# Performance work log

Measured on AMD Instinct MI355X. Metric: run time of the kernel, lower is better.

The kernel has to match this reference:

```python
import jax, jax.numpy as jnp
import numpy as np

B, S = 16, 4096
E_ENC, E_DEC, H = 1024, 1024, 512


def setup_inputs() -> dict:
    key = jax.random.key(0)
    ks = jax.random.split(key, 8)
    sc_e = 1.0 / np.sqrt(E_ENC)
    sc_d = 1.0 / np.sqrt(E_DEC)
    sc_h = 1.0 / np.sqrt(H)
    return {
        "encoder_hiddens": jax.random.normal(ks[0], (B, S, E_ENC), jnp.float32),
        "decoder_hidden": jax.random.normal(ks[1], (B, E_DEC), jnp.float32),
        "We": jax.random.uniform(ks[2], (E_ENC, H), jnp.float32, -sc_e, sc_e),
        "be": jax.random.uniform(ks[3], (H,), jnp.float32, -sc_e, sc_e),
        "Wd": jax.random.uniform(ks[4], (E_DEC, H), jnp.float32, -sc_d, sc_d),
        "bd": jax.random.uniform(ks[5], (H,), jnp.float32, -sc_d, sc_d),
        "Wo": jax.random.uniform(ks[6], (H, 1), jnp.float32, -sc_h, sc_h),
        "bo": jax.random.uniform(ks[7], (1,), jnp.float32, -sc_h, sc_h),
    }


def reference(encoder_hiddens, decoder_hidden, We, be, Wd, bd, Wo, bo):
    # Additive (Bahdanau) attention.
    # enc_proj: [B,S,H]; dec_proj: [B,1,H] broadcast over sequence.
    enc_proj = jnp.einsum("bse,eh->bsh", encoder_hiddens, We) + be
    dec_proj = jnp.einsum("bd,dh->bh", decoder_hidden, Wd) + bd
    e = jnp.tanh(enc_proj + dec_proj[:, None, :])          # [B,S,H]
    scores = jnp.einsum("bsh,h->bs", e, Wo[:, 0]) + bo[0]  # [B,S]
    attn = jax.nn.softmax(scores, axis=-1)                 # [B,S]
    context = jnp.einsum("bs,bse->be", attn, encoder_hiddens)  # [B,E_ENC]
    return context
```

## Files before the change

kernel.cpp:

```cpp
#include <hip/hip_runtime.h>
#include <hip/hip_bf16.h>
#include <math.h>

#define B_ 16
#define S_ 4096
#define E_ 1024
#define H_ 512

#define BM 128
#define BN 128
#define BK 64
#define NCHUNK (E_ / BK)

typedef short bf16x8 __attribute__((ext_vector_type(8)));
typedef unsigned short u16x8 __attribute__((ext_vector_type(8)));
typedef float f32x4 __attribute__((ext_vector_type(4)));

__device__ inline unsigned short f2bf(float x) {
    __hip_bfloat16 h = __float2bfloat16(x);
    return *(unsigned short*)&h;
}
__device__ inline float bf2f(unsigned short u) {
    unsigned int x = ((unsigned int)u) << 16;
    float f;
    __builtin_memcpy(&f, &x, 4);
    return f;
}
__device__ __forceinline__ void gld16(const unsigned short* g, unsigned short* l) {
    __builtin_amdgcn_global_load_lds(
        (const __attribute__((address_space(1))) void*)g,
        (__attribute__((address_space(3))) void*)l, 16, 0, 0);
}

__global__ __launch_bounds__(256) void prep_kernel(
    const float* __restrict__ We, const float* __restrict__ dec,
    const float* __restrict__ Wd, const float* __restrict__ bd,
    const float* __restrict__ be, unsigned short* __restrict__ WeTcB,
    float* __restrict__ dp) {
    __shared__ float red[4][64];
    int bid = blockIdx.x, t = threadIdx.x;
    if (bid < 64) {
        int c = bid >> 2, n0t = (bid & 3) * 128;
#pragma unroll 4
        for (int it = 0; it < 32; ++it) {
            int o = it * 256 + t;
            int n_rel = o >> 6, within = o & 63;
            int cp = within >> 3, j = within & 7;
            int n = n0t + n_rel;
            int k = c * 64 + ((cp ^ (n & 7)) << 3) + j;
            WeTcB[c * 32768 + n * 64 + within] = f2bf(We[(size_t)k * H_ + n]);
        }
    } else {
        int id = bid - 64;
        int b = id >> 3, hc = id & 7;
        int h = hc * 64 + (t & 63);
        int ec = t >> 6;
        const float* dr = dec + b * E_ + ec * 256;
        const float* wp = Wd + (size_t)(ec * 256) * H_ + h;
        float acc = 0.f;
#pragma unroll 8
        for (int e = 0; e < 256; ++e) acc = fmaf(dr[e], wp[(size_t)e * H_], acc);
        red[ec][t & 63] = acc;
        __syncthreads();
        if (t < 64) {
            int hh = hc * 64 + t;
            dp[b * H_ + hh] = red[0][t] + red[1][t] + red[2][t] + red[3][t] + bd[hh] + be[hh];
        }
    }
}

__global__ __launch_bounds__(256, 3) void scores_gemm_kernel(
    const float* __restrict__ enc, const unsigned short* __restrict__ WeTcB,
    const float* __restrict__ Wo, const float* __restrict__ dp,
    float* __restrict__ parts, unsigned short* __restrict__ encB) {
    __shared__ unsigned short sA[BM * BK];
    __shared__ unsigned short sB[BN * BK];
    __shared__ float sRed[2][BM];

    int tid = threadIdx.x;
    int w = tid >> 6, l = tid & 63;
    int l16 = l & 15, quad = l >> 4;
    int wm = w & 1, wn = w >> 1;
    int bid = blockIdx.x;
    int xcd = bid & 7;
    int sq = bid >> 3;
    int nt = sq & 3;
    size_t mt = (size_t)((sq >> 2) << 3) + xcd;
    size_t m0 = mt * BM;
    int n0 = nt * BN;
    int b = (int)(m0 >> 12);
    bool writeB = (nt == 0);

    int arowS = tid >> 3;
    int akb = tid & 7;
    const float* gAf = enc + (m0 + arowS) * E_ + akb * 8;
    unsigned short* sAw = sA + arowS * BK + ((akb ^ (arowS & 7)) << 3);
    unsigned short* encBw = encB + (m0 + arowS) * E_ + akb * 8;
    const unsigned short* gB = WeTcB + (size_t)n0 * BK + (w * 8) * BK + l * 8;
    unsigned short* sBb = sB + (w * 8) * BK;

    f32x4 acc[4][4];
#pragma unroll
    for (int i = 0; i < 4; ++i)
#pragma unroll
        for (int j = 0; j < 4; ++j) acc[i][j] = (f32x4)0.f;

    int arow = (wm * 64 + l16) * BK;
    int brow = (wn * 64 + l16) * BK;
    int sw = l16 & 7;

    for (int c = 0; c < NCHUNK; ++c) {
        __syncthreads();
        int k0 = c * BK;
#pragma unroll
        for (int i = 0; i < 4; ++i)
            gld16(gB + (size_t)c * (H_ * BK) + i * 32 * BK, sBb + i * 32 * BK);
#pragma unroll
        for (int it = 0; it < 4; ++it) {
            const float* p = gAf + (size_t)it * 32 * E_ + k0;
            float4 va = *(const float4*)(p);
            float4 vb = *(const float4*)(p + 4);
            u16x8 u;
            u[0] = f2bf(va.x); u[1] = f2bf(va.y); u[2] = f2bf(va.z); u[3] = f2bf(va.w);
            u[4] = f2bf(vb.x); u[5] = f2bf(vb.y); u[6] = f2bf(vb.z); u[7] = f2bf(vb.w);
            *(u16x8*)(sAw + it * 32 * BK) = u;
            if (writeB) *(u16x8*)(encBw + (size_t)it * 32 * E_ + k0) = u;
        }
        __syncthreads();
#pragma unroll
        for (int half = 0; half < 2; ++half) {
            int koff = (((half * 4 + quad) ^ sw) << 3);
            bf16x8 aR[4], bR[4];
#pragma unroll
            for (int i = 0; i < 4; ++i)
                aR[i] = *(const bf16x8*)(sA + arow + i * 16 * BK + koff);
#pragma unroll
            for (int j = 0; j < 4; ++j)
                bR[j] = *(const bf16x8*)(sB + brow + j * 16 * BK + koff);
#pragma unroll
            for (int i = 0; i < 4; ++i)
#pragma unroll
                for (int j = 0; j < 4; ++j)
                    acc[i][j] = __builtin_amdgcn_mfma_f32_16x16x32_bf16(aR[i], bR[j], acc[i][j], 0, 0, 0);
        }
    }

    float dpv[4], wov[4];
    const float* dpb = dp + b * H_;
#pragma unroll
    for (int j = 0; j < 4; ++j) {
        int h = n0 + wn * 64 + j * 16 + l16;
        dpv[j] = dpb[h];
        wov[j] = Wo[h];
    }
#pragma unroll
    for (int i = 0; i < 4; ++i)
#pragma unroll
        for (int r = 0; r < 4; ++r) {
            float s = 0.f;
#pragma unroll
            for (int j = 0; j < 4; ++j) {
                float x = acc[i][j][r] + dpv[j];
                float e = __expf(2.f * x);
                s += (1.f - 2.f / (e + 1.f)) * wov[j];
            }
            s += __shfl_xor(s, 1, 64);
            s += __shfl_xor(s, 2, 64);
            s += __shfl_xor(s, 4, 64);
            s += __shfl_xor(s, 8, 64);
            if (l16 == 0) sRed[wn][wm * 64 + i * 16 + quad * 4 + r] = s;
        }
    __syncthreads();
    if (tid < BM) {
        int s_in = (int)(m0 & (S_ - 1)) + tid;
        parts[(size_t)(nt * B_ + b) * S_ + s_in] = sRed[0][tid] + sRed[1][tid];
    }
}

__global__ __launch_bounds__(256) void stats_kernel(const float* __restrict__ parts,
                                                    float2* __restrict__ stats) {
    int b = blockIdx.x, tid = threadIdx.x;
    const float4* p0 = (const float4*)(parts + (size_t)(0 * B_ + b) * S_);
    const float4* p1 = (const float4*)(parts + (size_t)(1 * B_ + b) * S_);
    const float4* p2 = (const float4*)(parts + (size_t)(2 * B_ + b) * S_);
    const float4* p3 = (const float4*)(parts + (size_t)(3 * B_ + b) * S_);
    float4 v[4];
    float m = -1e30f;
#pragma unroll
    for (int i = 0; i < 4; ++i) {
        int idx = i * 256 + tid;
        float4 a0 = p0[idx], a1 = p1[idx], a2 = p2[idx], a3 = p3[idx];
        v[i].x = a0.x + a1.x + a2.x + a3.x;
        v[i].y = a0.y + a1.y + a2.y + a3.y;
        v[i].z = a0.z + a1.z + a2.z + a3.z;
        v[i].w = a0.w + a1.w + a2.w + a3.w;
        m = fmaxf(m, fmaxf(fmaxf(v[i].x, v[i].y), fmaxf(v[i].z, v[i].w)));
    }
    for (int off = 32; off; off >>= 1) m = fmaxf(m, __shfl_xor(m, off, 64));
    __shared__ float redm[4];
    __shared__ float reds[4];
    if ((tid & 63) == 0) redm[tid >> 6] = m;
    __syncthreads();
    m = fmaxf(fmaxf(redm[0], redm[1]), fmaxf(redm[2], redm[3]));
    float s = 0.f;
#pragma unroll
    for (int i = 0; i < 4; ++i) {
        s += __expf(v[i].x - m) + __expf(v[i].y - m);
        s += __expf(v[i].z - m) + __expf(v[i].w - m);
    }
    for (int off = 32; off; off >>= 1) s += __shfl_xor(s, off, 64);
    if ((tid & 63) == 0) reds[tid >> 6] = s;
    __syncthreads();
    if (tid == 0) {
        stats[b] = make_float2(m, reds[0] + reds[1] + reds[2] + reds[3]);
    }
}

__global__ __launch_bounds__(256) void ctx_partial_bf16(
    const unsigned short* __restrict__ encB, const float* __restrict__ parts,
    const float2* __restrict__ stats, float* __restrict__ part) {
    int b = blockIdx.x >> 5;
    int c = blockIdx.x & 31;
    int s0 = c * 128;
    int tid = threadIdx.x;
    __shared__ float w[128];
    if (tid < 128) {
        size_t idx = (size_t)b * S_ + s0 + tid;
        float x = parts[(size_t)(0 * B_) * S_ + idx] + parts[(size_t)(1 * B_) * S_ + idx] +
                  parts[(size_t)(2 * B_) * S_ + idx] + parts[(size_t)(3 * B_) * S_ + idx];
        w[tid] = __expf(x - stats[b].x);
    }
    __syncthreads();
    int e8 = (tid & 127) * 8;
    int sh = tid >> 7;
    const unsigned short* base = encB + ((size_t)b * S_ + s0 + sh * 64) * E_ + e8;
    const float* wp = w + sh * 64;
    float acc[8];
#pragma unroll
    for (int t = 0; t < 8; ++t) acc[t] = 0.f;
    for (int s = 0; s < 64; s += 8) {
        u16x8 v[8];
#pragma unroll
        for (int u = 0; u < 8; ++u) v[u] = *(const u16x8*)(base + (size_t)(s + u) * E_);
#pragma unroll
        for (int u = 0; u < 8; ++u) {
            float ws = wp[s + u];
#pragma unroll
            for (int t = 0; t < 8; ++t) acc[t] = fmaf(ws, bf2f(v[u][t]), acc[t]);
        }
    }
    float* po = part + ((size_t)(b * 64 + c * 2 + sh)) * E_ + e8;
    *(float4*)(po) = make_float4(acc[0], acc[1], acc[2], acc[3]);
    *(float4*)(po + 4) = make_float4(acc[4], acc[5], acc[6], acc[7]);
}

__global__ __launch_bounds__(256) void ctx_reduce(const float* __restrict__ part,
                                                  const float2* __restrict__ stats,
                                                  float* __restrict__ out) {
    int idx = blockIdx.x * 256 + threadIdx.x;
    int b = idx >> 10;
    int e = idx & 1023;
    const float* p = part + (size_t)b * 64 * E_ + e;
    float s0 = 0.f, s1 = 0.f, s2 = 0.f, s3 = 0.f;
    for (int c = 0; c < 64; c += 4) {
        s0 += p[(size_t)(c + 0) * E_];
        s1 += p[(size_t)(c + 1) * E_];
        s2 += p[(size_t)(c + 2) * E_];
        s3 += p[(size_t)(c + 3) * E_];
    }
    out[idx] = ((s0 + s1) + (s2 + s3)) * (1.f / stats[b].y);
}

extern "C" void kernel_launch(void* const* d_in, const int* in_sizes, int n_in,
                              void* d_out, int out_size, void* d_ws, size_t ws_size,
                              hipStream_t stream) {
    const float* enc = (const float*)d_in[0];
    const float* dec = (const float*)d_in[1];
    const float* We  = (const float*)d_in[2];
    const float* be  = (const float*)d_in[3];
    const float* Wd  = (const float*)d_in[4];
    const float* bd  = (const float*)d_in[5];
    const float* Wo  = (const float*)d_in[6];
    float* out = (float*)d_out;

    char* wsp = (char*)d_ws;
    unsigned short* WeTcB = (unsigned short*)wsp;
    float* dp = (float*)(wsp + (1 << 20));
    float2* stats = (float2*)(wsp + (1 << 20) + (32 << 10));
    float* parts = (float*)(wsp + (1 << 20) + (64 << 10));
    float* part = (float*)(wsp + (4 << 20));
    unsigned short* encB = (unsigned short*)(wsp + (8 << 20));

    prep_kernel<<<192, 256, 0, stream>>>(We, dec, Wd, bd, be, WeTcB, dp);
    scores_gemm_kernel<<<(B_ * S_ / BM) * (H_ / BN), 256, 0, stream>>>(
        enc, WeTcB, Wo, dp, parts, encB);
    stats_kernel<<<B_, 256, 0, stream>>>(parts, stats);
    ctx_partial_bf16<<<B_ * 32, 256, 0, stream>>>(encB, parts, stats, part);
    ctx_reduce<<<B_ * E_ / 256, 256, 0, stream>>>(part, stats, out);
}
```

Before: 514.2 us.

## Load fp32 encoder tiles directly to LDS, drop bf16 copy, fuse softmax stats

The GEMM now streams fp32 encoder tiles into LDS with global_load_lds, using an XOR-swizzled layout, and converts them to bf16 when reading fragments. This removes the register-staged conversion path and the bf16 side copy of the encoder. The context pass reads the fp32 encoder directly and computes per-chunk max and sum. The separate stats kernel is replaced by a chunked online-softmax rescale in ctx_reduce. The cost is double the LDS footprint for A, which may cut occupancy, and a second full fp32 read of the encoder in the context pass.

After: 489.3 us. 4.8% less time.

```diff
diff --git a/kernel.cpp b/kernel.cpp
--- a/kernel.cpp
+++ b/kernel.cpp
@@ -26,7 +26,7 @@
     __builtin_memcpy(&f, &x, 4);
     return f;
 }
-__device__ __forceinline__ void gld16(const unsigned short* g, unsigned short* l) {
+__device__ __forceinline__ void gld16(const void* g, void* l) {
     __builtin_amdgcn_global_load_lds(
         (const __attribute__((address_space(1))) void*)g,
         (__attribute__((address_space(3))) void*)l, 16, 0, 0);
@@ -72,8 +72,8 @@
 __global__ __launch_bounds__(256, 3) void scores_gemm_kernel(
     const float* __restrict__ enc, const unsigned short* __restrict__ WeTcB,
     const float* __restrict__ Wo, const float* __restrict__ dp,
-    float* __restrict__ parts, unsigned short* __restrict__ encB) {
-    __shared__ unsigned short sA[BM * BK];
+    float* __restrict__ parts) {
+    __shared__ float sAf[BM * BK];
     __shared__ unsigned short sB[BN * BK];
     __shared__ float sRed[2][BM];
 
@@ -89,13 +89,15 @@
     size_t m0 = mt * BM;
     int n0 = nt * BN;
     int b = (int)(m0 >> 12);
-    bool writeB = (nt == 0);
-
-    int arowS = tid >> 3;
-    int akb = tid & 7;
-    const float* gAf = enc + (m0 + arowS) * E_ + akb * 8;
-    unsigned short* sAw = sA + arowS * BK + ((akb ^ (arowS & 7)) << 3);
-    unsigned short* encBw = encB + (m0 + arowS) * E_ + akb * 8;
+
+    int arow_l = l >> 4;
+    int p32 = (l & 15) >> 1;
+    int half_l = l & 1;
+    int ge = (p32 ^ arow_l) * 8 + half_l * 4;
+    int go = (p32 ^ ((arow_l + 4) & 7)) * 8 + half_l * 4;
+    const float* gA_even = enc + (m0 + w * 32 + arow_l) * E_ + ge;
+    const float* gA_odd  = enc + (m0 + w * 32 + arow_l) * E_ + go;
+    float* sAf_w = sAf + (w * 32) * BK;
     const unsigned short* gB = WeTcB + (size_t)n0 * BK + (w * 8) * BK + l * 8;
     unsigned short* sBb = sB + (w * 8) * BK;
 
@@ -105,9 +107,9 @@
 #pragma unroll
         for (int j = 0; j < 4; ++j) acc[i][j] = (f32x4)0.f;
 
-    int arow = (wm * 64 + l16) * BK;
     int brow = (wn * 64 + l16) * BK;
     int sw = l16 & 7;
+    int arowf = (wm * 64 + l16) * BK;
 
     for (int c = 0; c < NCHUNK; ++c) {
         __syncthreads();
@@ -116,27 +118,29 @@
         for (int i = 0; i < 4; ++i)
             gld16(gB + (size_t)c * (H_ * BK) + i * 32 * BK, sBb + i * 32 * BK);
 #pragma unroll
-        for (int it = 0; it < 4; ++it) {
-            const float* p = gAf + (size_t)it * 32 * E_ + k0;
-            float4 va = *(const float4*)(p);
-            float4 vb = *(const float4*)(p + 4);
-            u16x8 u;
-            u[0] = f2bf(va.x); u[1] = f2bf(va.y); u[2] = f2bf(va.z); u[3] = f2bf(va.w);
-            u[4] = f2bf(vb.x); u[5] = f2bf(vb.y); u[6] = f2bf(vb.z); u[7] = f2bf(vb.w);
-            *(u16x8*)(sAw + it * 32 * BK) = u;
-            if (writeB) *(u16x8*)(encBw + (size_t)it * 32 * E_ + k0) = u;
+        for (int i = 0; i < 8; ++i) {
+            const float* src = ((i & 1) ? gA_odd : gA_even) + (size_t)i * 4 * E_ + k0;
+            gld16(src, sAf_w + i * 4 * BK);
         }
         __syncthreads();
 #pragma unroll
         for (int half = 0; half < 2; ++half) {
-            int koff = (((half * 4 + quad) ^ sw) << 3);
+            int kq = half * 4 + quad;
             bf16x8 aR[4], bR[4];
 #pragma unroll
-            for (int i = 0; i < 4; ++i)
-                aR[i] = *(const bf16x8*)(sA + arow + i * 16 * BK + koff);
+            for (int i = 0; i < 4; ++i) {
+                int phys = (kq ^ sw) * 8;
+                const float* ap = sAf + arowf + i * 16 * BK + phys;
+                f32x4 lo = *(const f32x4*)(ap);
+                f32x4 hi = *(const f32x4*)(ap + 4);
+                u16x8 u;
+                u[0] = f2bf(lo[0]); u[1] = f2bf(lo[1]); u[2] = f2bf(lo[2]); u[3] = f2bf(lo[3]);
+                u[4] = f2bf(hi[0]); u[5] = f2bf(hi[1]); u[6] = f2bf(hi[2]); u[7] = f2bf(hi[3]);
+                aR[i] = *(bf16x8*)&u;
+            }
 #pragma unroll
             for (int j = 0; j < 4; ++j)
-                bR[j] = *(const bf16x8*)(sB + brow + j * 16 * BK + koff);
+                bR[j] = *(const bf16x8*)(sB + brow + j * 16 * BK + ((kq ^ sw) << 3));
 #pragma unroll
             for (int i = 0; i < 4; ++i)
 #pragma unroll
@@ -177,77 +181,72 @@
     }
 }
 
-__global__ __launch_bounds__(256) void stats_kernel(const float* __restrict__ parts,
-                                                    float2* __restrict__ stats) {
-    int b = blockIdx.x, tid = threadIdx.x;
-    const float4* p0 = (const float4*)(parts + (size_t)(0 * B_ + b) * S_);
-    const float4* p1 = (const float4*)(parts + (size_t)(1 * B_ + b) * S_);
-    const float4* p2 = (const float4*)(parts + (size_t)(2 * B_ + b) * S_);
-    const float4* p3 = (const float4*)(parts + (size_t)(3 * B_ + b) * S_);
-    float4 v[4];
-    float m = -1e30f;
-#pragma unroll
-    for (int i = 0; i < 4; ++i) {
-        int idx = i * 256 + tid;
-        float4 a0 = p0[idx], a1 = p1[idx], a2 = p2[idx], a3 = p3[idx];
-        v[i].x = a0.x + a1.x + a2.x + a3.x;
-        v[i].y = a0.y + a1.y + a2.y + a3.y;
-        v[i].z = a0.z + a1.z + a2.z + a3.z;
-        v[i].w = a0.w + a1.w + a2.w + a3.w;
-        m = fmaxf(m, fmaxf(fmaxf(v[i].x, v[i].y), fmaxf(v[i].z, v[i].w)));
-    }
-    for (int off = 32; off; off >>= 1) m = fmaxf(m, __shfl_xor(m, off, 64));
-    __shared__ float redm[4];
-    __shared__ float reds[4];
-    if ((tid & 63) == 0) redm[tid >> 6] = m;
-    __syncthreads();
-    m = fmaxf(fmaxf(redm[0], redm[1]), fmaxf(redm[2], redm[3]));
-    float s = 0.f;
-#pragma unroll
-    for (int i = 0; i < 4; ++i) {
-        s += __expf(v[i].x - m) + __expf(v[i].y - m);
-        s += __expf(v[i].z - m) + __expf(v[i].w - m);
-    }
-    for (int off = 32; off; off >>= 1) s += __shfl_xor(s, off, 64);
-    if ((tid & 63) == 0) reds[tid >> 6] = s;
-    __syncthreads();
-    if (tid == 0) {
-        stats[b] = make_float2(m, reds[0] + reds[1] + reds[2] + reds[3]);
-    }
-}
-
-__global__ __launch_bounds__(256) void ctx_partial_bf16(
-    const unsigned short* __restrict__ encB, const float* __restrict__ parts,
-    const float2* __restrict__ stats, float* __restrict__ part) {
+__global__ __launch_bounds__(256) void ctx_partial_f32(
+    const float* __restrict__ enc, const float* __restrict__ parts,
+    float* __restrict__ part, float2* __restrict__ statsC) {
     int b = blockIdx.x >> 5;
     int c = blockIdx.x & 31;
     int s0 = c * 128;
     int tid = threadIdx.x;
     __shared__ float w[128];
+    __shared__ float redm[2], redz[2];
+    float sc = -1e30f;
     if (tid < 128) {
         size_t idx = (size_t)b * S_ + s0 + tid;
-        float x = parts[(size_t)(0 * B_) * S_ + idx] + parts[(size_t)(1 * B_) * S_ + idx] +
-                  parts[(size_t)(2 * B_) * S_ + idx] + parts[(size_t)(3 * B_) * S_ + idx];
-        w[tid] = __expf(x - stats[b].x);
-    }
-    __syncthreads();
+        sc = parts[(size_t)(0 * B_) * S_ + idx] + parts[(size_t)(1 * B_) * S_ + idx] +
+             parts[(size_t)(2 * B_) * S_ + idx] + parts[(size_t)(3 * B_) * S_ + idx];
+        w[tid] = sc;
+    }
+    __syncthreads();
+    float m = sc;
+    for (int off = 32; off; off >>= 1) m = fmaxf(m, __shfl_xor(m, off, 64));
+    if (tid < 128 && (tid & 63) == 0) redm[tid >> 6] = m;
+    __syncthreads();
+    float mc = fmaxf(redm[0], redm[1]);
+    float z = 0.f;
+    if (tid < 128) {
+        float e = __expf(w[tid] - mc);
+        z = e;
+        w[tid] = e;
+    }
+    for (int off = 32; off; off >>= 1) z += __shfl_xor(z, off, 64);
+    if (tid < 128 && (tid & 63) == 0) redz[tid >> 6] = z;
+    __syncthreads();
+    if (tid == 0) statsC[b * 32 + c] = make_float2(mc, redz[0] + redz[1]);
+
     int e8 = (tid & 127) * 8;
     int sh = tid >> 7;
-    const unsigned short* base = encB + ((size_t)b * S_ + s0 + sh * 64) * E_ + e8;
+    const float* base = enc + ((size_t)b * S_ + s0 + sh * 64) * E_ + e8;
     const float* wp = w + sh * 64;
     float acc[8];
 #pragma unroll
     for (int t = 0; t < 8; ++t) acc[t] = 0.f;
-    for (int s = 0; s < 64; s += 8) {
-        u16x8 v[8];
-#pragma unroll
-        for (int u = 0; u < 8; ++u) v[u] = *(const u16x8*)(base + (size_t)(s + u) * E_);
-#pragma unroll
-        for (int u = 0; u < 8; ++u) {
-            float ws = wp[s + u];
-#pragma unroll
-            for (int t = 0; t < 8; ++t) acc[t] = fmaf(ws, bf2f(v[u][t]), acc[t]);
-        }
+    for (int s = 0; s < 64; s += 4) {
+        float4 v0a = *(const float4*)(base + (size_t)(s + 0) * E_);
+        float4 v0b = *(const float4*)(base + (size_t)(s + 0) * E_ + 4);
+        float4 v1a = *(const float4*)(base + (size_t)(s + 1) * E_);
+        float4 v1b = *(const float4*)(base + (size_t)(s + 1) * E_ + 4);
+        float4 v2a = *(const float4*)(base + (size_t)(s + 2) * E_);
+        float4 v2b = *(const float4*)(base + (size_t)(s + 2) * E_ + 4);
+        float4 v3a = *(const float4*)(base + (size_t)(s + 3) * E_);
+        float4 v3b = *(const float4*)(base + (size_t)(s + 3) * E_ + 4);
+        float w0 = wp[s], w1 = wp[s + 1], w2 = wp[s + 2], w3 = wp[s + 3];
+        acc[0] = fmaf(w0, v0a.x, acc[0]); acc[1] = fmaf(w0, v0a.y, acc[1]);
+        acc[2] = fmaf(w0, v0a.z, acc[2]); acc[3] = fmaf(w0, v0a.w, acc[3]);
+        acc[4] = fmaf(w0, v0b.x, acc[4]); acc[5] = fmaf(w0, v0b.y, acc[5]);
+        acc[6] = fmaf(w0, v0b.z, acc[6]); acc[7] = fmaf(w0, v0b.w, acc[7]);
+        acc[0] = fmaf(w1, v1a.x, acc[0]); acc[1] = fmaf(w1, v1a.y, acc[1]);
+        acc[2] = fmaf(w1, v1a.z, acc[2]); acc[3] = fmaf(w1, v1a.w, acc[3]);
+        acc[4] = fmaf(w1, v1b.x, acc[4]); acc[5] = fmaf(w1, v1b.y, acc[5]);
+        acc[6] = fmaf(w1, v1b.z, acc[6]); acc[7] = fmaf(w1, v1b.w, acc[7]);
+        acc[0] = fmaf(w2, v2a.x, acc[0]); acc[1] = fmaf(w2, v2a.y, acc[1]);
+        acc[2] = fmaf(w2, v2a.z, acc[2]); acc[3] = fmaf(w2, v2a.w, acc[3]);
+        acc[4] = fmaf(w2, v2b.x, acc[4]); acc[5] = fmaf(w2, v2b.y, acc[5]);
+        acc[6] = fmaf(w2, v2b.z, acc[6]); acc[7] = fmaf(w2, v2b.w, acc[7]);
+        acc[0] = fmaf(w3, v3a.x, acc[0]); acc[1] = fmaf(w3, v3a.y, acc[1]);
+        acc[2] = fmaf(w3, v3a.z, acc[2]); acc[3] = fmaf(w3, v3a.w, acc[3]);
+        acc[4] = fmaf(w3, v3b.x, acc[4]); acc[5] = fmaf(w3, v3b.y, acc[5]);
+        acc[6] = fmaf(w3, v3b.z, acc[6]); acc[7] = fmaf(w3, v3b.w, acc[7]);
     }
     float* po = part + ((size_t)(b * 64 + c * 2 + sh)) * E_ + e8;
     *(float4*)(po) = make_float4(acc[0], acc[1], acc[2], acc[3]);
@@ -255,20 +254,38 @@
 }
 
 __global__ __launch_bounds__(256) void ctx_reduce(const float* __restrict__ part,
-                                                  const float2* __restrict__ stats,
+                                                  const float2* __restrict__ statsC,
                                                   float* __restrict__ out) {
-    int idx = blockIdx.x * 256 + threadIdx.x;
-    int b = idx >> 10;
-    int e = idx & 1023;
+    int b = blockIdx.x >> 2;
+    int e = (blockIdx.x & 3) * 256 + threadIdx.x;
+    __shared__ float ef[32];
+    if (threadIdx.x == 0) {
+        float M = -1e30f;
+        float2 st[32];
+#pragma unroll 8
+        for (int c = 0; c < 32; ++c) {
+            st[c] = statsC[b * 32 + c];
+            M = fmaxf(M, st[c].x);
+        }
+        float Z = 0.f;
+#pragma unroll 8
+        for (int c = 0; c < 32; ++c) ef[c] = __expf(st[c].x - M);
+#pragma unroll 8
+        for (int c = 0; c < 32; ++c) Z += st[c].y * ef[c];
+        float inv = 1.f / Z;
+#pragma unroll 8
+        for (int c = 0; c < 32; ++c) ef[c] *= inv;
+    }
+    __syncthreads();
     const float* p = part + (size_t)b * 64 * E_ + e;
     float s0 = 0.f, s1 = 0.f, s2 = 0.f, s3 = 0.f;
-    for (int c = 0; c < 64; c += 4) {
-        s0 += p[(size_t)(c + 0) * E_];
-        s1 += p[(size_t)(c + 1) * E_];
-        s2 += p[(size_t)(c + 2) * E_];
-        s3 += p[(size_t)(c + 3) * E_];
-    }
-    out[idx] = ((s0 + s1) + (s2 + s3)) * (1.f / stats[b].y);
+    for (int sl = 0; sl < 64; sl += 4) {
+        s0 += p[(size_t)(sl + 0) * E_] * ef[(sl + 0) >> 1];
+        s1 += p[(size_t)(sl + 1) * E_] * ef[(sl + 1) >> 1];
+        s2 += p[(size_t)(sl + 2) * E_] * ef[(sl + 2) >> 1];
+        s3 += p[(size_t)(sl + 3) * E_] * ef[(sl + 3) >> 1];
+    }
+    out[(size_t)b * E_ + e] = (s0 + s1) + (s2 + s3);
 }
 
 extern "C" void kernel_launch(void* const* d_in, const int* in_sizes, int n_in,
@@ -286,15 +303,13 @@
     char* wsp = (char*)d_ws;
     unsigned short* WeTcB = (unsigned short*)wsp;
     float* dp = (float*)(wsp + (1 << 20));
-    float2* stats = (float2*)(wsp + (1 << 20) + (32 << 10));
+    float2* statsC = (float2*)(wsp + (1 << 20) + (32 << 10));
     float* parts = (float*)(wsp + (1 << 20) + (64 << 10));
     float* part = (float*)(wsp + (4 << 20));
-    unsigned short* encB = (unsigned short*)(wsp + (8 << 20));
 
     prep_kernel<<<192, 256, 0, stream>>>(We, dec, Wd, bd, be, WeTcB, dp);
     scores_gemm_kernel<<<(B_ * S_ / BM) * (H_ / BN), 256, 0, stream>>>(
-        enc, WeTcB, Wo, dp, parts, encB);
-    stats_kernel<<<B_, 256, 0, stream>>>(parts, stats);
-    ctx_partial_bf16<<<B_ * 32, 256, 0, stream>>>(encB, parts, stats, part);
-    ctx_reduce<<<B_ * E_ / 256, 256, 0, stream>>>(part, stats, out);
-}
+        enc, WeTcB, Wo, dp, parts);
+    ctx_partial_f32<<<B_ * 32, 256, 0, stream>>>(enc, parts, part, statsC);
+    ctx_reduce<<<B_ * 4, 256, 0, stream>>>(part, statsC, out);
+}
```
